# Kernel tuning notes

Hardware: AMD Instinct MI355X
Metric: run time of the kernel (lower is better)

The kernel has to match this reference:

```python
import jax, jax.numpy as jnp
import numpy as np

B, S_IMG, S_TXT, H, D = 1, 2048, 512, 24, 128
HID = H * D  # 3072
S_TOT = S_TXT + S_IMG
IP_SCALE = 1.0
EPS = 1e-5


def setup_inputs() -> dict:
    key = jax.random.key(0)
    ks = jax.random.split(key, 16)
    r = lambda k, s: jax.random.normal(k, s, dtype=jnp.float32)
    w = lambda k, s: r(k, s) * 0.02
    theta = r(ks[15], (S_TOT, D))  # rotary angles over joint sequence
    z = lambda: jnp.zeros((HID,), jnp.float32)
    return dict(
        hidden_states=r(ks[0], (B, S_IMG, HID)),
        encoder_hidden_states=r(ks[1], (B, S_TXT, HID)),
        image_emb=r(ks[2], (B, 4, HID)),
        rope_cos=jnp.cos(theta), rope_sin=jnp.sin(theta),
        Wq=w(ks[3], (HID, HID)), bq=z(),
        Wk=w(ks[4], (HID, HID)), bk=z(),
        Wv=w(ks[5], (HID, HID)), bv=z(),
        Waq=w(ks[6], (HID, HID)), baq=z(),
        Wak=w(ks[7], (HID, HID)), bak=z(),
        Wav=w(ks[8], (HID, HID)), bav=z(),
        Wk_ip=w(ks[9], (HID, HID)),
        Wv_ip=w(ks[10], (HID, HID)),
        Wo=w(ks[11], (HID, HID)), bo=z(),
        Wao=w(ks[12], (HID, HID)), bao=z(),
    )


def _heads(x):  # [B,S,HID] -> [B,H,S,D]
    return x.reshape(x.shape[0], x.shape[1], H, D).transpose(0, 2, 1, 3)


def _unheads(x):  # [B,H,S,D] -> [B,S,HID]
    return x.transpose(0, 2, 1, 3).reshape(x.shape[0], x.shape[2], HID)


def _rmsnorm(x):  # over last dim, no affine (RMSNorm(128, affine=False))
    return x * jax.lax.rsqrt(jnp.mean(x * x, axis=-1, keepdims=True) + EPS)


def _rope(x, cos, sin):  # diffusers apply_rotary_emb, use_real, interleaved pairs
    xp = x.reshape(*x.shape[:-1], D // 2, 2)
    rot = jnp.stack([-xp[..., 1], xp[..., 0]], axis=-1).reshape(x.shape)
    return x * cos + rot * sin  # cos/sin [S,D] broadcast over [B,H,S,D]


def _sdpa(q, k, v):
    s = jnp.einsum('bhqd,bhkd->bhqk', q, k) / jnp.sqrt(jnp.asarray(D, q.dtype))
    return jnp.einsum('bhqk,bhkd->bhqd', jax.nn.softmax(s, axis=-1), v)


def _forward(hidden_states, encoder_hidden_states, image_emb, rope_cos, rope_sin,
             Wq, bq, Wk, bk, Wv, bv, Waq, baq, Wak, bak, Wav, bav,
             Wk_ip, Wv_ip, Wo, bo, Wao, bao):
    # main QKV over image-latent tokens
    q = _rmsnorm(_heads(hidden_states @ Wq.T + bq))
    k = _rmsnorm(_heads(hidden_states @ Wk.T + bk))
    v = _heads(hidden_states @ Wv.T + bv)
    # IP-adapter cross attention (query = latent q, kv from image_emb)
    k_ip = _rmsnorm(_heads(image_emb @ Wk_ip.T))
    v_ip = _heads(image_emb @ Wv_ip.T)
    ip_out = _unheads(_sdpa(q, k_ip, v_ip))  # [B,S_IMG,HID]
    # encoder (text) QKV, concat text-first as in Flux
    eq = _rmsnorm(_heads(encoder_hidden_states @ Waq.T + baq))
    ek = _rmsnorm(_heads(encoder_hidden_states @ Wak.T + bak))
    ev = _heads(encoder_hidden_states @ Wav.T + bav)
    q = jnp.concatenate([eq, q], axis=2)
    k = jnp.concatenate([ek, k], axis=2)
    v = jnp.concatenate([ev, v], axis=2)
    q = _rope(q, rope_cos, rope_sin)
    k = _rope(k, rope_cos, rope_sin)
    out = _unheads(_sdpa(q, k, v))  # [B,S_TOT,HID]
    enc_out, hid_out = out[:, :S_TXT], out[:, S_TXT:]
    hid_out = hid_out + IP_SCALE * ip_out
    hid_out = hid_out @ Wo.T + bo   # to_out[0] (+ identity dropout)
    enc_out = enc_out @ Wao.T + bao  # to_add_out
    return hid_out, enc_out


def reference(hidden_states, encoder_hidden_states, image_emb, rope_cos, rope_sin,
              Wq, bq, Wk, bk, Wv, bv, Waq, baq, Wak, bak, Wav, bav,
              Wk_ip, Wv_ip, Wo, bo, Wao, bao):
    return _forward(hidden_states, encoder_hidden_states, image_emb, rope_cos, rope_sin,
                    Wq, bq, Wk, bk, Wv, bv, Waq, baq, Wak, bak, Wav, bav,
                    Wk_ip, Wv_ip, Wo, bo, Wao, bao)
```

## Files before the change

kernel.cpp:

```cpp
#include <hip/hip_runtime.h>

typedef __bf16 bf16;
typedef __bf16 bf16x2 __attribute__((ext_vector_type(2)));
typedef __bf16 bf16x4 __attribute__((ext_vector_type(4)));
typedef __bf16 bf16x8 __attribute__((ext_vector_type(8)));
typedef float  f32x4  __attribute__((ext_vector_type(4)));

#define H_    24
#define D_    128
#define HID_  3072
#define SIMG_ 2048
#define STXT_ 512
#define STOT_ 2560
#define EPS_  1e-5f
#define SCALE_ 0.08838834764831845f
#define HH_   ((size_t)HID_*HID_)

typedef __attribute__((address_space(3))) unsigned int lds_uint;
typedef const __attribute__((address_space(1))) unsigned int glb_uint;
__device__ __forceinline__ void gll16(const void* g, void* l){
  __builtin_amdgcn_global_load_lds((glb_uint*)g, (lds_uint*)l, 16, 0, 0);
}

__device__ inline bf16x8 frag8f(const float* __restrict__ p){
  const f32x4 a = *(const f32x4*)p;
  const f32x4 b = *(const f32x4*)(p + 4);
  bf16x8 r;
  r[0]=(bf16)a[0]; r[1]=(bf16)a[1]; r[2]=(bf16)a[2]; r[3]=(bf16)a[3];
  r[4]=(bf16)b[0]; r[5]=(bf16)b[1]; r[6]=(bf16)b[2]; r[7]=(bf16)b[3];
  return r;
}

__device__ __forceinline__ void cvt8(const float* __restrict__ s, bf16* __restrict__ d, int i){
  const f32x4 a = *(const f32x4*)(s + i);
  const f32x4 b = *(const f32x4*)(s + i + 4);
  bf16x8 o;
  o[0]=(bf16)a[0]; o[1]=(bf16)a[1]; o[2]=(bf16)a[2]; o[3]=(bf16)a[3];
  o[4]=(bf16)b[0]; o[5]=(bf16)b[1]; o[6]=(bf16)b[2]; o[7]=(bf16)b[3];
  *(bf16x8*)(d + i) = o;
}

#define CONV_BLK 2048
__global__ __launch_bounds__(256) void k_prep(
    const float* __restrict__ HS, const float* __restrict__ ENC,
    const float* __restrict__ W0, const float* __restrict__ W1,
    const float* __restrict__ W2, const float* __restrict__ W3,
    const float* __restrict__ W4, const float* __restrict__ W5,
    const float* __restrict__ W6, const float* __restrict__ W7,
    const float* __restrict__ IMG,
    const float* __restrict__ Wkip, const float* __restrict__ Wvip,
    bf16* __restrict__ HSb, bf16* __restrict__ ENCb, bf16* __restrict__ Wb8,
    float* __restrict__ Kip, float* __restrict__ Vip)
{
  __shared__ float tile[4][128];
  const int bx = (int)blockIdx.x;
  const int t = (int)threadIdx.x;
  if (bx < 48){
    const bool isV = (bx >= 24);
    const int h = bx % 24;
    const float* Wm = isV ? Wvip : Wkip;
    const int w = t >> 6, l = t & 63;
    const int lr = l & 15, lg = l >> 4;
    const int col0 = h*128 + w*32;
    f32x4 acc0 = {}, acc1 = {};
    const float* arow = IMG + (size_t)((lr < 4) ? lr : 0)*HID_;
    const float* wr0 = Wm + (size_t)(col0 + lr)*HID_;
    const float* wr1 = Wm + (size_t)(col0 + 16 + lr)*HID_;
    for (int k0 = 0; k0 < HID_; k0 += 32){
      const bf16x8 af = frag8f(arow + k0 + lg*8);
      acc0 = __builtin_amdgcn_mfma_f32_16x16x32_bf16(af, frag8f(wr0 + k0 + lg*8), acc0, 0, 0, 0);
      acc1 = __builtin_amdgcn_mfma_f32_16x16x32_bf16(af, frag8f(wr1 + k0 + lg*8), acc1, 0, 0, 0);
    }
    if (lg == 0){
      #pragma unroll
      for (int r = 0; r < 4; r++){
        tile[r][w*32 + lr]      = acc0[r];
        tile[r][w*32 + 16 + lr] = acc1[r];
      }
    }
    __syncthreads();
    if (isV){
      const int e = t*2;
      const int j = e >> 7, d = e & 127;
      Vip[(size_t)(h*4 + j)*D_ + d]     = tile[j][d];
      Vip[(size_t)(h*4 + j)*D_ + d + 1] = tile[j][d + 1];
    } else {
      const float v0 = tile[w][2*l], v1 = tile[w][2*l + 1];
      float ss = v0*v0 + v1*v1;
      #pragma unroll
      for (int m = 1; m < 64; m <<= 1) ss += __shfl_xor(ss, m);
      const float rk = rsqrtf(ss*(1.0f/128.0f) + EPS_);
      Kip[(size_t)(h*4 + w)*D_ + 2*l]     = v0*rk;
      Kip[(size_t)(h*4 + w)*D_ + 2*l + 1] = v1*rk;
    }
  } else {
    for (int c = bx - 48; c < 20352; c += CONV_BLK){
      const float* s; bf16* d; int base;
      if (c < 1536){ s = HS;  d = HSb;  base = c*4096; }
      else if (c < 1920){ s = ENC; d = ENCb; base = (c - 1536)*4096; }
      else {
        const int idx = c - 1920;
        const int wi = idx / 2304;
        s = (wi==0)?W0:(wi==1)?W1:(wi==2)?W2:(wi==3)?W3:(wi==4)?W4:(wi==5)?W5:(wi==6)?W6:W7;
        d = Wb8 + (size_t)wi*HH_;
        base = (idx % 2304)*4096;
      }
      const int i = base + t*16;
      cvt8(s, d, i);
      cvt8(s, d, i + 8);
    }
  }
}

#define MFMA_ __builtin_amdgcn_mfma_f32_16x16x32_bf16
#define MM(bfr, n) \
    acc[0][n]=MFMA_(af0,bfr,acc[0][n],0,0,0); acc[1][n]=MFMA_(af1,bfr,acc[1][n],0,0,0); \
    acc[2][n]=MFMA_(af2,bfr,acc[2][n],0,0,0); acc[3][n]=MFMA_(af3,bfr,acc[3][n],0,0,0);
#define WAIT6  asm volatile("s_waitcnt vmcnt(6)" ::: "memory")
#define WAIT0  asm volatile("s_waitcnt vmcnt(0)" ::: "memory")
#define NOWAIT (void)0

__device__ __forceinline__ void gemm8_core(
    const bf16* __restrict__ A, const bf16* __restrict__ W,
    int mb, int nb,
    f32x4 (&acc)[4][4],
    bf16 (&Al)[3][128][64],
    bf16 (&Bl)[3][256][64])
{
  const int t = (int)threadIdx.x;
  const int w = t >> 6, l = t & 63;
  const int lr = l & 15, lg = l >> 4;
  const int wr = w >> 2, wc = w & 3;
  const int srow = t >> 3;
  const int soff = ((t & 7) ^ (srow & 7)) * 8;

  const bf16* Abase = A + (size_t)(mb + srow)*HID_ + soff;
  const bf16* Wbase = W + (size_t)(nb + srow)*HID_ + soff;

#define SA(buf, tt, i) gll16(Abase + (size_t)(i)*64*HID_ + (tt)*64, &Al[buf][0][0] + (i)*4096 + t*8)
#define SB(buf, tt, i) gll16(Wbase + (size_t)(i)*64*HID_ + (tt)*64, &Bl[buf][0][0] + (i)*4096 + t*8)

  const int arow_ = wr*64 + lr;
  const int brow_ = wc*64 + lr;
  const int sx = lr & 7;

  SA(0,0,0); SA(0,0,1); SB(0,0,0); SB(0,0,1); SB(0,0,2); SB(0,0,3);
  SA(1,1,0); SA(1,1,1); SB(1,1,0); SB(1,1,1); SB(1,1,2); SB(1,1,3);
  WAIT6;
  __builtin_amdgcn_s_barrier();

#define TILE(C, NXT, TT, PRE, TW)                                            \
  {                                                                          \
    const int s0_ = (lg^sx)*8, s1_ = ((4+lg)^sx)*8;                          \
    bf16x8 af0,af1,af2,af3,b0,b1;                                            \
    af0=*(const bf16x8*)&Al[C][arow_   ][s0_];                               \
    af1=*(const bf16x8*)&Al[C][arow_+16][s0_];                               \
    af2=*(const bf16x8*)&Al[C][arow_+32][s0_];                               \
    af3=*(const bf16x8*)&Al[C][arow_+48][s0_];                               \
    b0 =*(const bf16x8*)&Bl[C][brow_   ][s0_];                               \
    b1 =*(const bf16x8*)&Bl[C][brow_+16][s0_];                               \
    if (PRE){ SA(NXT,(TT)+2,0); SA(NXT,(TT)+2,1); }                          \
    __builtin_amdgcn_s_setprio(1); MM(b0,0) MM(b1,1)                         \
    __builtin_amdgcn_s_setprio(0);                                           \
    b0 =*(const bf16x8*)&Bl[C][brow_+32][s0_];                               \
    b1 =*(const bf16x8*)&Bl[C][brow_+48][s0_];                               \
    if (PRE){ SB(NXT,(TT)+2,0); SB(NXT,(TT)+2,1); }                          \
    __builtin_amdgcn_s_setprio(1); MM(b0,2) MM(b1,3)                         \
    __builtin_amdgcn_s_setprio(0);                                           \
    af0=*(const bf16x8*)&Al[C][arow_   ][s1_];                               \
    af1=*(const bf16x8*)&Al[C][arow_+16][s1_];                               \
    af2=*(const bf16x8*)&Al[C][arow_+32][s1_];                               \
    af3=*(const bf16x8*)&Al[C][arow_+48][s1_];                               \
    b0 =*(const bf16x8*)&Bl[C][brow_   ][s1_];                               \
    b1 =*(const bf16x8*)&Bl[C][brow_+16][s1_];                               \
    if (PRE){ SB(NXT,(TT)+2,2); SB(NXT,(TT)+2,3); }                          \
    __builtin_amdgcn_s_setprio(1); MM(b0,0) MM(b1,1)                         \
    __builtin_amdgcn_s_setprio(0);                                           \
    b0 =*(const bf16x8*)&Bl[C][brow_+32][s1_];                               \
    b1 =*(const bf16x8*)&Bl[C][brow_+48][s1_];                               \
    __builtin_amdgcn_s_setprio(1); MM(b0,2) MM(b1,3)                         \
    __builtin_amdgcn_s_setprio(0);                                           \
    TW;                                                                      \
    __builtin_amdgcn_s_barrier();                                            \
  }

  for (int base = 0; base < 45; base += 3){
    TILE(0, 2, base,   true, WAIT6);
    TILE(1, 0, base+1, true, WAIT6);
    TILE(2, 1, base+2, true, WAIT6);
  }
  TILE(0, 2, 45, true,  WAIT6);
  TILE(1, 0, 46, false, WAIT0);
  TILE(2, 1, 47, false, NOWAIT);
#undef TILE
#undef SA
#undef SB
}

__global__ __launch_bounds__(512, 1) void k_gemm8_qkv(
    const bf16* __restrict__ Ahid, const bf16* __restrict__ Aenc,
    const bf16* __restrict__ Wb,
    const float* bq, const float* bk, const float* bv,
    const float* baq, const float* bak, const float* bav,
    bf16* Cq, bf16* Ck, bf16* Cv, bf16* Ceq, bf16* Cek, bf16* Cev)
{
  __shared__ __align__(16) bf16 Al[3][128][64];
  __shared__ __align__(16) bf16 Bl[3][256][64];
  const int lin = (int)blockIdx.x;
  const int work = (lin & 7)*90 + (lin >> 3);
  const int mt = work / 36;
  const int ct = work % 36;
  const int which = ct % 3;
  const int nb = (ct/3)*256;
  const int enc = (mt >= 16) ? 1 : 0;
  const int mb = (enc ? (mt - 16) : mt)*128;
  const bf16* A = enc ? Aenc : Ahid;
  const int widx = which + enc*3;
  const bf16* W = Wb + (size_t)widx*HH_;
  const float* bias = (which==0) ? (enc?baq:bq) : (which==1) ? (enc?bak:bk) : (enc?bav:bv);
  bf16* Cm = (which==0) ? (enc?Ceq:Cq) : (which==1) ? (enc?Cek:Ck) : (enc?Cev:Cv);

  f32x4 acc[4][4] = {};
  gemm8_core(A, W, mb, nb, acc, Al, Bl);

  const int w = (int)(threadIdx.x >> 6), l = (int)(threadIdx.x & 63u);
  const int lr = l & 15, lg = l >> 4;
  const int wr = w >> 2, wc = w & 3;
  #pragma unroll
  for (int nf = 0; nf < 4; nf++){
    const int col = nb + wc*64 + nf*16 + lr;
    const float bvl = bias[col];
    #pragma unroll
    for (int m = 0; m < 4; m++){
      #pragma unroll
      for (int r = 0; r < 4; r++){
        const int row = mb + wr*64 + m*16 + lg*4 + r;
        Cm[(size_t)row*HID_ + col] = (bf16)(acc[m][nf][r] + bvl);
      }
    }
  }
}

__global__ __launch_bounds__(512, 1) void k_gemm8_out(
    const bf16* __restrict__ Ahid, const bf16* __restrict__ Aenc,
    const bf16* __restrict__ Wb,
    const float* bo, const float* bao, float* __restrict__ outp)
{
  __shared__ __align__(16) bf16 Al[3][128][64];
  __shared__ __align__(16) bf16 Bl[3][256][64];
  const int lin = (int)blockIdx.x;
  const int work = (lin & 7)*30 + (lin >> 3);
  const int mt = work / 12;
  const int nb = (work % 12)*256;
  const int enc = (mt >= 16) ? 1 : 0;
  const int mb = (enc ? (mt - 16) : mt)*128;
  const bf16* A = enc ? Aenc : Ahid;
  const bf16* W = Wb + (size_t)(enc ? 7 : 6)*HH_;
  const float* bias = enc ? bao : bo;
  float* C = outp + (enc ? (size_t)SIMG_*HID_ : 0);

  f32x4 acc[4][4] = {};
  gemm8_core(A, W, mb, nb, acc, Al, Bl);

  const int w = (int)(threadIdx.x >> 6), l = (int)(threadIdx.x & 63u);
  const int lr = l & 15, lg = l >> 4;
  const int wr = w >> 2, wc = w & 3;
  #pragma unroll
  for (int nf = 0; nf < 4; nf++){
    const int col = nb + wc*64 + nf*16 + lr;
    const float bvl = bias[col];
    #pragma unroll
    for (int m = 0; m < 4; m++){
      #pragma unroll
      for (int r = 0; r < 4; r++){
        const int row = mb + wr*64 + m*16 + lg*4 + r;
        C[(size_t)row*HID_ + col] = acc[m][nf][r] + bvl;
      }
    }
  }
}

#define FIN_BLK 2048
__global__ __launch_bounds__(256) void k_finish_qk2(
    const bf16* __restrict__ rawQ, const bf16* __restrict__ rawK,
    const bf16* __restrict__ rawEQ, const bf16* __restrict__ rawEK,
    const float* __restrict__ cosT, const float* __restrict__ sinT,
    const float* __restrict__ Kip, const float* __restrict__ Vip,
    bf16* __restrict__ Qh, bf16* __restrict__ Kh, bf16* __restrict__ ipOut)
{
  const int wv = (int)(threadIdx.x >> 6);
  const int l = (int)(threadIdx.x & 63u);
  const int d0 = 2*l, d1 = 2*l + 1;
  for (int b = (int)blockIdx.x; b < 15360; b += FIN_BLK){
    const int wid = b*4 + wv;
    const int s = wid / H_;
    const int h = wid % H_;
    const bf16 *sq_, *sk_;
    if (s < STXT_){
      const size_t off = (size_t)s*HID_ + h*D_;
      sq_ = rawEQ + off; sk_ = rawEK + off;
    } else {
      const size_t off = (size_t)(s - STXT_)*HID_ + h*D_;
      sq_ = rawQ + off; sk_ = rawK + off;
    }
    float q0 = sq_[d0], q1 = sq_[d1];
    float k0 = sk_[d0], k1 = sk_[d1];
    float ssq = q0*q0 + q1*q1;
    float ssk = k0*k0 + k1*k1;
    #pragma unroll
    for (int m = 1; m < 64; m <<= 1){ ssq += __shfl_xor(ssq, m); ssk += __shfl_xor(ssk, m); }
    const float rq = rsqrtf(ssq*(1.0f/128.0f) + EPS_);
    const float rk = rsqrtf(ssk*(1.0f/128.0f) + EPS_);
    q0 *= rq; q1 *= rq; k0 *= rk; k1 *= rk;
    const float c0 = cosT[(size_t)s*D_ + d0], c1 = cosT[(size_t)s*D_ + d1];
    const float s0 = sinT[(size_t)s*D_ + d0], s1 = sinT[(size_t)s*D_ + d1];
    const float qo0 = q0*c0 - q1*s0, qo1 = q1*c1 + q0*s1;
    const float ko0 = k0*c0 - k1*s0, ko1 = k1*c1 + k0*s1;
    const size_t qoff = ((size_t)h*STOT_ + s)*D_ + d0;
    Qh[qoff] = (bf16)qo0; Qh[qoff + 1] = (bf16)qo1;
    Kh[qoff] = (bf16)ko0; Kh[qoff + 1] = (bf16)ko1;

    if (s >= STXT_){
      const float* kb = Kip + (size_t)h*4*D_;
      const float* vb = Vip + (size_t)h*4*D_;
      float sc[4];
      #pragma unroll
      for (int j = 0; j < 4; j++) sc[j] = q0*kb[j*D_ + d0] + q1*kb[j*D_ + d1];
      #pragma unroll
      for (int m = 1; m < 64; m <<= 1){
        #pragma unroll
        for (int j = 0; j < 4; j++) sc[j] += __shfl_xor(sc[j], m);
      }
      const float mx = fmaxf(fmaxf(sc[0], sc[1]), fmaxf(sc[2], sc[3]));
      float p[4], ps = 0.f;
      #pragma unroll
      for (int j = 0; j < 4; j++){ p[j] = __expf((sc[j] - mx)*SCALE_); ps += p[j]; }
      const float inv = 1.0f/ps;
      float o0 = 0.f, o1 = 0.f;
      #pragma unroll
      for (int j = 0; j < 4; j++){ o0 += p[j]*vb[j*D_ + d0]; o1 += p[j]*vb[j*D_ + d1]; }
      const size_t dst = (size_t)(s - STXT_)*HID_ + h*D_;
      ipOut[dst + d0] = (bf16)(o0*inv);
      ipOut[dst + d1] = (bf16)(o1*inv);
    }
  }
}

__global__ __launch_bounds__(256) void k_vtrans(
    const bf16* __restrict__ rawV, const bf16* __restrict__ rawEV,
    bf16* __restrict__ Vt)
{
  __shared__ bf16 lt[128*130];
  const int t = (int)threadIdx.x;
  const int stile = (int)blockIdx.x*128;
  const int h = (int)blockIdx.y;
  #pragma unroll
  for (int i = 0; i < 8; i++){
    const int sl = i*16 + (t >> 4);
    const int s = stile + sl;
    const bf16* src = (s < STXT_) ? (rawEV + (size_t)s*HID_) : (rawV + (size_t)(s - STXT_)*HID_);
    const bf16x8 v = *(const bf16x8*)(src + h*D_ + (t & 15)*8);
    #pragma unroll
    for (int j = 0; j < 8; j++) lt[((t & 15)*8 + j)*130 + sl] = v[j];
  }
  __syncthreads();
  #pragma unroll
  for (int j = 0; j < 4; j++){
    const int d = j*32 + (t >> 3);
    const int s0 = (t & 7)*16;
    bf16x8 a, b;
    #pragma unroll
    for (int k = 0; k < 4; k++){
      const bf16x2 p = *(const bf16x2*)(lt + d*130 + s0 + 2*k);
      a[2*k] = p[0]; a[2*k+1] = p[1];
    }
    #pragma unroll
    for (int k = 0; k < 4; k++){
      const bf16x2 p = *(const bf16x2*)(lt + d*130 + s0 + 8 + 2*k);
      b[2*k] = p[0]; b[2*k+1] = p[1];
    }
    bf16* dst = Vt + ((size_t)h*D_ + d)*STOT_ + stile + s0;
    *(bf16x8*)dst = a;
    *(bf16x8*)(dst + 8) = b;
  }
}

__global__ __launch_bounds__(256, 2) void k_flash3(
    const bf16* __restrict__ Q, const bf16* __restrict__ K,
    const bf16* __restrict__ Vt, const bf16* __restrict__ ipOut,
    bf16* __restrict__ attnOut)
{
  __shared__ __align__(16) bf16 Ks[2][64*128];
  __shared__ __align__(16) bf16 Vs[2][128*64];
  __shared__ __align__(16) bf16 plds[4][32*64];
  const int t = (int)threadIdx.x;
  const int w = t >> 6, l = t & 63;
  const int lr = l & 15, lg = l >> 4;
  const int lin = (int)blockIdx.x;
  const int work = (lin & 7)*60 + (lin >> 3);
  const int h = work / 20;
  const int qbase = (work % 20)*128 + w*32;
  const bf16* Qh = Q  + (size_t)h*STOT_*D_;
  const bf16* Kh = K  + (size_t)h*STOT_*D_;
  const bf16* Vh = Vt + (size_t)h*D_*STOT_;

  bf16x8 qf[2][4];
  #pragma unroll
  for (int qt = 0; qt < 2; qt++)
    #pragma unroll
    for (int kk = 0; kk < 4; kk++)
      qf[qt][kk] = *(const bf16x8*)(Qh + (size_t)(qbase + qt*16 + lr)*D_ + kk*32 + lg*8);

  f32x4 acc[2][8] = {};
  float mrun[2] = {-3.0e38f, -3.0e38f}, lrun[2] = {0.f, 0.f};

  const int krow = t >> 4, kslot = t & 15;
  const int vrow = t >> 3, vslot = t & 7;

  auto STAGE = [&](int buf, int kv){
    #pragma unroll
    for (int i = 0; i < 4; i++){
      const int r = i*16 + krow;
      gll16(Kh + (size_t)(kv + r)*D_ + ((kslot ^ (r & 7))*8),
            (void*)(&Ks[buf][0] + (size_t)t*8 + i*2048));
    }
    #pragma unroll
    for (int i = 0; i < 4; i++){
      const int r = i*32 + vrow;
      gll16(Vh + (size_t)r*STOT_ + kv + ((vslot ^ (r & 7))*8),
            (void*)(&Vs[buf][0] + (size_t)t*8 + i*2048));
    }
  };

  STAGE(0, 0);
  __syncthreads();
  int cur = 0;
  for (int kv = 0; kv < STOT_; kv += 64){
    if (kv + 64 < STOT_) STAGE(cur ^ 1, kv + 64);

    f32x4 st[2][4] = {};
    #pragma unroll
    for (int tt = 0; tt < 4; tt++){
      const int kr = tt*16 + lr;
      #pragma unroll
      for (int kk = 0; kk < 4; kk++){
        const bf16x8 kf = *(const bf16x8*)(&Ks[cur][0] + kr*128 + (((kk*4 + lg) ^ (kr & 7))*8));
        st[0][tt] = __builtin_amdgcn_mfma_f32_16x16x32_bf16(kf, qf[0][kk], st[0][tt], 0, 0, 0);
        st[1][tt] = __builtin_amdgcn_mfma_f32_16x16x32_bf16(kf, qf[1][kk], st[1][tt], 0, 0, 0);
      }
    }
    #pragma unroll
    for (int qt = 0; qt < 2; qt++){
      const int q = qt*16 + lr;
      float sv[4][4];
      float vmax = -3.0e38f;
      #pragma unroll
      for (int tt = 0; tt < 4; tt++)
        #pragma unroll
        for (int r = 0; r < 4; r++){ const float x = st[qt][tt][r]*SCALE_; sv[tt][r] = x; vmax = fmaxf(vmax, x); }
      vmax = fmaxf(vmax, __shfl_xor(vmax, 16));
      vmax = fmaxf(vmax, __shfl_xor(vmax, 32));
      const bool grow = __any(vmax > mrun[qt] + 8.0f);
      float mnew = mrun[qt];
      if (grow){
        mnew = fmaxf(mrun[qt], vmax);
        const float alpha = __expf(mrun[qt] - mnew);
        lrun[qt] *= alpha;
        #pragma unroll
        for (int n = 0; n < 8; n++)
          #pragma unroll
          for (int r = 0; r < 4; r++) acc[qt][n][r] *= alpha;
        mrun[qt] = mnew;
      }
      float rs = 0.f;
      #pragma unroll
      for (int tt = 0; tt < 4; tt++){
        bf16x4 pq;
        #pragma unroll
        for (int r = 0; r < 4; r++){
          const float p = __expf(sv[tt][r] - mnew);
          rs += p;
          pq[r] = (bf16)p;
        }
        *(bf16x4*)(&plds[w][q*64 + (((tt*2 + (lg >> 1)) ^ (q & 7))*8) + (lg & 1)*4]) = pq;
      }
      rs += __shfl_xor(rs, 16);
      rs += __shfl_xor(rs, 32);
      lrun[qt] += rs;
    }
    #pragma unroll
    for (int ks = 0; ks < 2; ks++){
      const bf16x8 pb0 = *(const bf16x8*)(&plds[w][(lr)*64      + (((ks*4 + lg) ^ (lr & 7))*8)]);
      const bf16x8 pb1 = *(const bf16x8*)(&plds[w][(16 + lr)*64 + (((ks*4 + lg) ^ (lr & 7))*8)]);
      #pragma unroll
      for (int n = 0; n < 8; n++){
        const int vr = n*16 + lr;
        const bf16x8 vf = *(const bf16x8*)(&Vs[cur][0] + vr*64 + (((ks*4 + lg) ^ (vr & 7))*8));
        acc[0][n] = __builtin_amdgcn_mfma_f32_16x16x32_bf16(vf, pb0, acc[0][n], 0, 0, 0);
        acc[1][n] = __builtin_amdgcn_mfma_f32_16x16x32_bf16(vf, pb1, acc[1][n], 0, 0, 0);
      }
    }
    __syncthreads();
    cur ^= 1;
  }
  const bool hid = (qbase >= STXT_);
  #pragma unroll
  for (int qt = 0; qt < 2; qt++){
    const float inv = 1.0f/lrun[qt];
    const int row = qbase + qt*16 + lr;
    #pragma unroll
    for (int n = 0; n < 8; n++){
      const size_t cbase = (size_t)row*HID_ + h*D_ + n*16 + lg*4;
      if (hid){
        const bf16x4 ip = *(const bf16x4*)(ipOut + (size_t)(row - STXT_)*HID_ + h*D_ + n*16 + lg*4);
        bf16x4 o;
        #pragma unroll
        for (int r = 0; r < 4; r++) o[r] = (bf16)(acc[qt][n][r]*inv + (float)ip[r]);
        *(bf16x4*)(attnOut + cbase) = o;
      } else {
        bf16x4 o;
        #pragma unroll
        for (int r = 0; r < 4; r++) o[r] = (bf16)(acc[qt][n][r]*inv);
        *(bf16x4*)(attnOut + cbase) = o;
      }
    }
  }
}

extern "C" void kernel_launch(void* const* d_in, const int* in_sizes, int n_in,
                              void* d_out, int out_size, void* d_ws, size_t ws_size,
                              hipStream_t stream)
{
  const float* HS   = (const float*)d_in[0];
  const float* ENC  = (const float*)d_in[1];
  const float* IMG  = (const float*)d_in[2];
  const float* COS  = (const float*)d_in[3];
  const float* SIN  = (const float*)d_in[4];
  const float* Wq   = (const float*)d_in[5];  const float* bq  = (const float*)d_in[6];
  const float* Wk   = (const float*)d_in[7];  const float* bk  = (const float*)d_in[8];
  const float* Wv   = (const float*)d_in[9];  const float* bv  = (const float*)d_in[10];
  const float* Waq  = (const float*)d_in[11]; const float* baq = (const float*)d_in[12];
  const float* Wak  = (const float*)d_in[13]; const float* bak = (const float*)d_in[14];
  const float* Wav  = (const float*)d_in[15]; const float* bav = (const float*)d_in[16];
  const float* Wkip = (const float*)d_in[17]; const float* Wvip= (const float*)d_in[18];
  const float* Wo   = (const float*)d_in[19]; const float* bo  = (const float*)d_in[20];
  const float* Wao  = (const float*)d_in[21]; const float* bao = (const float*)d_in[22];

  char* wsb = (char*)d_ws;
  size_t off = 0;
  auto alloc = [&](size_t bytes) -> char* {
    char* p = wsb + off; off += (bytes + 255) & ~((size_t)255); return p;
  };
  bf16* rawQ   = (bf16*)alloc((size_t)SIMG_*HID_*2);
  bf16* rawK   = (bf16*)alloc((size_t)SIMG_*HID_*2);
  bf16* rawV   = (bf16*)alloc((size_t)SIMG_*HID_*2);
  bf16* rawEQ  = (bf16*)alloc((size_t)STXT_*HID_*2);
  bf16* rawEK  = (bf16*)alloc((size_t)STXT_*HID_*2);
  bf16* rawEV  = (bf16*)alloc((size_t)STXT_*HID_*2);
  bf16* Qb     = (bf16*)alloc((size_t)H_*STOT_*D_*2);
  bf16* Kb     = (bf16*)alloc((size_t)H_*STOT_*D_*2);
  bf16* Vtb    = (bf16*)alloc((size_t)H_*STOT_*D_*2);
  bf16* AOUT   = (bf16*)alloc((size_t)STOT_*HID_*2);
  bf16* IPOUT  = (bf16*)alloc((size_t)SIMG_*HID_*2);
  float* KIPF  = (float*)alloc((size_t)H_*4*D_*4);
  float* VIPF  = (float*)alloc((size_t)H_*4*D_*4);
  bf16* HSb    = (bf16*)alloc((size_t)SIMG_*HID_*2);
  bf16* ENCb   = (bf16*)alloc((size_t)STXT_*HID_*2);
  bf16* Wb8    = (bf16*)alloc((size_t)8*HH_*2);

  dim3 blk(256);
  dim3 blk512(512);
  k_prep<<<dim3(48 + CONV_BLK), blk, 0, stream>>>(HS, ENC, Wq, Wk, Wv, Waq, Wak, Wav, Wo, Wao,
                                                  IMG, Wkip, Wvip, HSb, ENCb, Wb8, KIPF, VIPF);
  k_gemm8_qkv<<<dim3(720), blk512, 0, stream>>>(HSb, ENCb, Wb8,
                                                bq, bk, bv, baq, bak, bav,
                                                rawQ, rawK, rawV, rawEQ, rawEK, rawEV);
  k_finish_qk2<<<dim3(FIN_BLK), blk, 0, stream>>>(rawQ, rawK, rawEQ, rawEK, COS, SIN,
                                                  KIPF, VIPF, Qb, Kb, IPOUT);
  k_vtrans<<<dim3(20,24), blk, 0, stream>>>(rawV, rawEV, Vtb);
  k_flash3<<<dim3(480), blk, 0, stream>>>(Qb, Kb, Vtb, IPOUT, AOUT);
  float* outp = (float*)d_out;
  k_gemm8_out<<<dim3(240), blk512, 0, stream>>>(AOUT + (size_t)STXT_*HID_, AOUT, Wb8, bo, bao, outp);
}
```

Measured before the change: 534.1 us.

## Replace QKV GEMM with 128x192 tile, 256-thread, two-blocks-per-CU kernel

Replaces the 512-thread 128x256-tile QKV projection GEMM with a new 256-thread kernel that computes 128x192 tiles using a 32-wide K step, a triple-buffered LDS pipeline and a new swizzled LDS layout. The grid becomes 960 blocks with two blocks per CU, so the tile count divides more evenly across CUs and occupancy rises. Each wave holds a 64x96 accumulator, which adds register pressure, and the shorter K step doubles the number of barriers per tile.

```diff
diff --git a/kernel.cpp b/kernel.cpp
--- a/kernel.cpp
+++ b/kernel.cpp
@@ -113,12 +113,127 @@
 }
 
 #define MFMA_ __builtin_amdgcn_mfma_f32_16x16x32_bf16
+#define WAIT6  asm volatile("s_waitcnt vmcnt(6)" ::: "memory")
+#define WAIT5  asm volatile("s_waitcnt vmcnt(5)" ::: "memory")
+#define WAIT0  asm volatile("s_waitcnt vmcnt(0)" ::: "memory")
+#define NOWAIT (void)0
+
+__global__ __launch_bounds__(256, 2) void k_gemm192_qkv(
+    const bf16* __restrict__ Ahid, const bf16* __restrict__ Aenc,
+    const bf16* __restrict__ Wb,
+    const float* bq, const float* bk, const float* bv,
+    const float* baq, const float* bak, const float* bav,
+    bf16* Cq, bf16* Ck, bf16* Cv, bf16* Ceq, bf16* Cek, bf16* Cev)
+{
+  __shared__ __align__(16) bf16 Al[3][4096];
+  __shared__ __align__(16) bf16 Bl[3][6144];
+  const int t = (int)threadIdx.x;
+  const int w = t >> 6, l = t & 63;
+  const int lr = l & 15, lg = l >> 4;
+  const int wr = w >> 1, wc = w & 1;
+
+  const int lin = (int)blockIdx.x;
+  const int work = (lin & 7)*120 + (lin >> 3);
+  const int mt = work / 48;
+  const int ct = work % 48;
+  const int which = ct % 3;
+  const int nb = (ct/3)*192;
+  const int enc = (mt >= 16) ? 1 : 0;
+  const int mb = (enc ? (mt - 16) : mt)*128;
+  const bf16* A = enc ? Aenc : Ahid;
+  const int widx = which + enc*3;
+  const bf16* W = Wb + (size_t)widx*HH_;
+  const float* bias = (which==0) ? (enc?baq:bq) : (which==1) ? (enc?bak:bk) : (enc?bav:bv);
+  bf16* Cm = (which==0) ? (enc?Ceq:Cq) : (which==1) ? (enc?Cek:Ck) : (enc?Cev:Cv);
+
+  const int lA0 = t >> 3,          uA0 = (t & 7) ^ (lA0 & 7);
+  const int gA1 = t + 256, lA1 = gA1 >> 3, uA1 = (gA1 & 7) ^ (lA1 & 7);
+  const bf16* Asrc0 = A + (size_t)(mb + 2*lA0 + (uA0 >> 2))*HID_ + (uA0 & 3)*8;
+  const bf16* Asrc1 = A + (size_t)(mb + 2*lA1 + (uA1 >> 2))*HID_ + (uA1 & 3)*8;
+  const int lB0 = t >> 3,          uB0 = (t & 7) ^ (lB0 & 7);
+  const int gB1 = t + 256, lB1 = gB1 >> 3, uB1 = (gB1 & 7) ^ (lB1 & 7);
+  const int gB2 = t + 512, lB2 = gB2 >> 3, uB2 = (gB2 & 7) ^ (lB2 & 7);
+  const bf16* Bsrc0 = W + (size_t)(nb + 2*lB0 + (uB0 >> 2))*HID_ + (uB0 & 3)*8;
+  const bf16* Bsrc1 = W + (size_t)(nb + 2*lB1 + (uB1 >> 2))*HID_ + (uB1 & 3)*8;
+  const bf16* Bsrc2 = W + (size_t)(nb + 2*lB2 + (uB2 >> 2))*HID_ + (uB2 & 3)*8;
+
+#define SA192(buf, TT) { gll16(Asrc0 + (TT)*32, &Al[buf][0] + t*8); \
+                         gll16(Asrc1 + (TT)*32, &Al[buf][0] + 2048 + t*8); }
+#define SB192(buf, TT) { gll16(Bsrc0 + (TT)*32, &Bl[buf][0] + t*8); \
+                         gll16(Bsrc1 + (TT)*32, &Bl[buf][0] + 2048 + t*8); \
+                         gll16(Bsrc2 + (TT)*32, &Bl[buf][0] + 4096 + t*8); }
+
+  const int gx = ((((lr & 1) << 2) | lg) ^ ((lr >> 1) & 7)) * 8;
+  const int baseA = (wr*32 + (lr >> 1))*64 + gx;
+  const int baseB = (wc*48 + (lr >> 1))*64 + gx;
+
+  f32x4 acc[4][6] = {};
+
+#define MMB(bb, n) \
+    acc[0][n]=MFMA_(a0,bb,acc[0][n],0,0,0); acc[1][n]=MFMA_(a1,bb,acc[1][n],0,0,0); \
+    acc[2][n]=MFMA_(a2,bb,acc[2][n],0,0,0); acc[3][n]=MFMA_(a3,bb,acc[3][n],0,0,0);
+
+#define TILE192(C, NXT, TT, PRE, TW)                                         \
+  {                                                                          \
+    bf16x8 a0,a1,a2,a3,b0,b1,b2;                                             \
+    a0 = *(const bf16x8*)(&Al[C][0] + baseA);                                \
+    a1 = *(const bf16x8*)(&Al[C][0] + baseA + 512);                          \
+    a2 = *(const bf16x8*)(&Al[C][0] + baseA + 1024);                         \
+    a3 = *(const bf16x8*)(&Al[C][0] + baseA + 1536);                         \
+    b0 = *(const bf16x8*)(&Bl[C][0] + baseB);                                \
+    b1 = *(const bf16x8*)(&Bl[C][0] + baseB + 512);                          \
+    b2 = *(const bf16x8*)(&Bl[C][0] + baseB + 1024);                         \
+    if (PRE){ SA192(NXT, (TT)+2); }                                          \
+    __builtin_amdgcn_s_setprio(1);                                           \
+    MMB(b0,0) MMB(b1,1) MMB(b2,2)                                            \
+    __builtin_amdgcn_s_setprio(0);                                           \
+    b0 = *(const bf16x8*)(&Bl[C][0] + baseB + 1536);                         \
+    b1 = *(const bf16x8*)(&Bl[C][0] + baseB + 2048);                         \
+    b2 = *(const bf16x8*)(&Bl[C][0] + baseB + 2560);                         \
+    if (PRE){ SB192(NXT, (TT)+2); }                                          \
+    __builtin_amdgcn_s_setprio(1);                                           \
+    MMB(b0,3) MMB(b1,4) MMB(b2,5)                                            \
+    __builtin_amdgcn_s_setprio(0);                                           \
+    TW;                                                                      \
+    __builtin_amdgcn_s_barrier();                                            \
+  }
+
+  SA192(0,0); SB192(0,0);
+  SA192(1,1); SB192(1,1);
+  WAIT5;
+  __builtin_amdgcn_s_barrier();
+
+  for (int base = 0; base < 93; base += 3){
+    TILE192(0, 2, base,   true, WAIT5);
+    TILE192(1, 0, base+1, true, WAIT5);
+    TILE192(2, 1, base+2, true, WAIT5);
+  }
+  TILE192(0, 2, 93, true,  WAIT5);
+  TILE192(1, 0, 94, false, WAIT0);
+  TILE192(2, 1, 95, false, NOWAIT);
+#undef TILE192
+#undef MMB
+#undef SA192
+#undef SB192
+
+  #pragma unroll
+  for (int n = 0; n < 6; n++){
+    const int col = nb + wc*96 + n*16 + lr;
+    const float bvl = bias[col];
+    #pragma unroll
+    for (int m = 0; m < 4; m++){
+      #pragma unroll
+      for (int r = 0; r < 4; r++){
+        const int row = mb + wr*64 + m*16 + lg*4 + r;
+        Cm[(size_t)row*HID_ + col] = (bf16)(acc[m][n][r] + bvl);
+      }
+    }
+  }
+}
+
 #define MM(bfr, n) \
     acc[0][n]=MFMA_(af0,bfr,acc[0][n],0,0,0); acc[1][n]=MFMA_(af1,bfr,acc[1][n],0,0,0); \
     acc[2][n]=MFMA_(af2,bfr,acc[2][n],0,0,0); acc[3][n]=MFMA_(af3,bfr,acc[3][n],0,0,0);
-#define WAIT6  asm volatile("s_waitcnt vmcnt(6)" ::: "memory")
-#define WAIT0  asm volatile("s_waitcnt vmcnt(0)" ::: "memory")
-#define NOWAIT (void)0
 
 __device__ __forceinline__ void gemm8_core(
     const bf16* __restrict__ A, const bf16* __restrict__ W,
@@ -197,50 +312,6 @@
 #undef SB
 }
 
-__global__ __launch_bounds__(512, 1) void k_gemm8_qkv(
-    const bf16* __restrict__ Ahid, const bf16* __restrict__ Aenc,
-    const bf16* __restrict__ Wb,
-    const float* bq, const float* bk, const float* bv,
-    const float* baq, const float* bak, const float* bav,
-    bf16* Cq, bf16* Ck, bf16* Cv, bf16* Ceq, bf16* Cek, bf16* Cev)
-{
-  __shared__ __align__(16) bf16 Al[3][128][64];
-  __shared__ __align__(16) bf16 Bl[3][256][64];
-  const int lin = (int)blockIdx.x;
-  const int work = (lin & 7)*90 + (lin >> 3);
-  const int mt = work / 36;
-  const int ct = work % 36;
-  const int which = ct % 3;
-  const int nb = (ct/3)*256;
-  const int enc = (mt >= 16) ? 1 : 0;
-  const int mb = (enc ? (mt - 16) : mt)*128;
-  const bf16* A = enc ? Aenc : Ahid;
-  const int widx = which + enc*3;
-  const bf16* W = Wb + (size_t)widx*HH_;
-  const float* bias = (which==0) ? (enc?baq:bq) : (which==1) ? (enc?bak:bk) : (enc?bav:bv);
-  bf16* Cm = (which==0) ? (enc?Ceq:Cq) : (which==1) ? (enc?Cek:Ck) : (enc?Cev:Cv);
-
-  f32x4 acc[4][4] = {};
-  gemm8_core(A, W, mb, nb, acc, Al, Bl);
-
-  const int w = (int)(threadIdx.x >> 6), l = (int)(threadIdx.x & 63u);
-  const int lr = l & 15, lg = l >> 4;
-  const int wr = w >> 2, wc = w & 3;
-  #pragma unroll
-  for (int nf = 0; nf < 4; nf++){
-    const int col = nb + wc*64 + nf*16 + lr;
-    const float bvl = bias[col];
-    #pragma unroll
-    for (int m = 0; m < 4; m++){
-      #pragma unroll
-      for (int r = 0; r < 4; r++){
-        const int row = mb + wr*64 + m*16 + lg*4 + r;
-        Cm[(size_t)row*HID_ + col] = (bf16)(acc[m][nf][r] + bvl);
-      }
-    }
-  }
-}
-
 __global__ __launch_bounds__(512, 1) void k_gemm8_out(
     const bf16* __restrict__ Ahid, const bf16* __restrict__ Aenc,
     const bf16* __restrict__ Wb,
@@ -572,9 +643,9 @@
   dim3 blk512(512);
   k_prep<<<dim3(48 + CONV_BLK), blk, 0, stream>>>(HS, ENC, Wq, Wk, Wv, Waq, Wak, Wav, Wo, Wao,
                                                   IMG, Wkip, Wvip, HSb, ENCb, Wb8, KIPF, VIPF);
-  k_gemm8_qkv<<<dim3(720), blk512, 0, stream>>>(HSb, ENCb, Wb8,
-                                                bq, bk, bv, baq, bak, bav,
-                                                rawQ, rawK, rawV, rawEQ, rawEK, rawEV);
+  k_gemm192_qkv<<<dim3(960), blk, 0, stream>>>(HSb, ENCb, Wb8,
+                                               bq, bk, bv, baq, bak, bav,
+                                               rawQ, rawK, rawV, rawEQ, rawEK, rawEV);
   k_finish_qk2<<<dim3(FIN_BLK), blk, 0, stream>>>(rawQ, rawK, rawEQ, rawEK, COS, SIN,
                                                   KIPF, VIPF, Qb, Kb, IPOUT);
   k_vtrans<<<dim3(20,24), blk, 0, stream>>>(rawV, rawEV, Vtb);
```

After: 513.0 us (median of 2 runs). -3.9%, faster.

## Replace QKV GEMM with 256x192 tile, 4-wave kernel and larger per-wave accumulators

Applied to the files above, without the earlier changes.

The QKV projection GEMM now uses a new kernel with 256x192 output tiles, 256 threads (4 waves) and a 128x96 per-wave accumulator block (8x6 MFMA tiles), replacing the 128x256 tile, 512-thread kernel. K is consumed in 32-wide steps with a triple-buffered global_load_lds pipeline and a new swizzled LDS layout. The larger per-wave tile raises arithmetic intensity per LDS read and cuts global traffic per FLOP. In exchange it uses far more accumulator registers, launches 480 blocks instead of 720 (fewer than two waves of blocks over the CUs), and runs twice as many barrier-synchronised K steps.

```diff
diff --git a/kernel.cpp b/kernel.cpp
--- a/kernel.cpp
+++ b/kernel.cpp
@@ -113,12 +113,136 @@
 }
 
 #define MFMA_ __builtin_amdgcn_mfma_f32_16x16x32_bf16
+#define WAIT7  asm volatile("s_waitcnt vmcnt(7)" ::: "memory")
+#define WAIT6  asm volatile("s_waitcnt vmcnt(6)" ::: "memory")
+#define WAIT0  asm volatile("s_waitcnt vmcnt(0)" ::: "memory")
+#define NOWAIT (void)0
+
+__global__ __launch_bounds__(256, 1) void k_gemm256x192_qkv(
+    const bf16* __restrict__ Ahid, const bf16* __restrict__ Aenc,
+    const bf16* __restrict__ Wb,
+    const float* bq, const float* bk, const float* bv,
+    const float* baq, const float* bak, const float* bav,
+    bf16* Cq, bf16* Ck, bf16* Cv, bf16* Ceq, bf16* Cek, bf16* Cev)
+{
+  __shared__ __align__(16) bf16 Al[3][8192];
+  __shared__ __align__(16) bf16 Bl[3][6144];
+  const int t = (int)threadIdx.x;
+  const int w = t >> 6, l = t & 63;
+  const int lr = l & 15, lg = l >> 4;
+  const int wr = w >> 1, wc = w & 1;
+
+  const int lin = (int)blockIdx.x;
+  const int work = (lin & 7)*60 + (lin >> 3);
+  const int mt = work / 48;
+  const int ct = work % 48;
+  const int which = ct % 3;
+  const int nb = (ct/3)*192;
+  const int enc = (mt >= 8) ? 1 : 0;
+  const int mb = (enc ? (mt - 8) : mt)*256;
+  const bf16* A = enc ? Aenc : Ahid;
+  const int widx = which + enc*3;
+  const bf16* W = Wb + (size_t)widx*HH_;
+  const float* bias = (which==0) ? (enc?baq:bq) : (which==1) ? (enc?bak:bk) : (enc?bav:bv);
+  bf16* Cm = (which==0) ? (enc?Ceq:Cq) : (which==1) ? (enc?Cek:Ck) : (enc?Cev:Cv);
+
+  const bf16* Asrc[4];
+  const bf16* Bsrc[3];
+  #pragma unroll
+  for (int i = 0; i < 4; i++){
+    const int gd = t + 256*i, ln = gd >> 3, u = (gd & 7) ^ (ln & 7);
+    Asrc[i] = A + (size_t)(mb + 2*ln + (u >> 2))*HID_ + (u & 3)*8;
+  }
+  #pragma unroll
+  for (int i = 0; i < 3; i++){
+    const int gd = t + 256*i, ln = gd >> 3, u = (gd & 7) ^ (ln & 7);
+    Bsrc[i] = W + (size_t)(nb + 2*ln + (u >> 2))*HID_ + (u & 3)*8;
+  }
+
+#define SAQ(buf, TT) { gll16(Asrc[0] + (TT)*32, &Al[buf][0] + t*8); \
+                       gll16(Asrc[1] + (TT)*32, &Al[buf][0] + 2048 + t*8); \
+                       gll16(Asrc[2] + (TT)*32, &Al[buf][0] + 4096 + t*8); \
+                       gll16(Asrc[3] + (TT)*32, &Al[buf][0] + 6144 + t*8); }
+#define SBQ(buf, TT) { gll16(Bsrc[0] + (TT)*32, &Bl[buf][0] + t*8); \
+                       gll16(Bsrc[1] + (TT)*32, &Bl[buf][0] + 2048 + t*8); \
+                       gll16(Bsrc[2] + (TT)*32, &Bl[buf][0] + 4096 + t*8); }
+
+  const int gx = ((((lr & 1) << 2) | lg) ^ ((lr >> 1) & 7)) * 8;
+  const int baseA = (wr*64 + (lr >> 1))*64 + gx;
+  const int baseB = (wc*48 + (lr >> 1))*64 + gx;
+
+  f32x4 acc[8][6] = {};
+
+#define MM6(am, m) \
+    acc[m][0]=MFMA_(am,b0,acc[m][0],0,0,0); acc[m][1]=MFMA_(am,b1,acc[m][1],0,0,0); \
+    acc[m][2]=MFMA_(am,b2,acc[m][2],0,0,0); acc[m][3]=MFMA_(am,b3,acc[m][3],0,0,0); \
+    acc[m][4]=MFMA_(am,b4,acc[m][4],0,0,0); acc[m][5]=MFMA_(am,b5,acc[m][5],0,0,0);
+
+#define TILEQ(C, TT, PRE, TW)                                                \
+  {                                                                          \
+    bf16x8 a0,a1,a2,a3,b0,b1,b2,b3,b4,b5;                                    \
+    a0 = *(const bf16x8*)(&Al[C][0] + baseA);                                \
+    a1 = *(const bf16x8*)(&Al[C][0] + baseA + 512);                          \
+    a2 = *(const bf16x8*)(&Al[C][0] + baseA + 1024);                         \
+    a3 = *(const bf16x8*)(&Al[C][0] + baseA + 1536);                         \
+    b0 = *(const bf16x8*)(&Bl[C][0] + baseB);                                \
+    b1 = *(const bf16x8*)(&Bl[C][0] + baseB + 512);                          \
+    b2 = *(const bf16x8*)(&Bl[C][0] + baseB + 1024);                         \
+    b3 = *(const bf16x8*)(&Bl[C][0] + baseB + 1536);                         \
+    b4 = *(const bf16x8*)(&Bl[C][0] + baseB + 2048);                         \
+    b5 = *(const bf16x8*)(&Bl[C][0] + baseB + 2560);                         \
+    if (PRE){ SAQ(((C)+2)%3, (TT)+2); }                                      \
+    __builtin_amdgcn_s_setprio(1);                                           \
+    MM6(a0,0) MM6(a1,1) MM6(a2,2) MM6(a3,3)                                  \
+    __builtin_amdgcn_s_setprio(0);                                           \
+    a0 = *(const bf16x8*)(&Al[C][0] + baseA + 2048);                         \
+    a1 = *(const bf16x8*)(&Al[C][0] + baseA + 2560);                         \
+    a2 = *(const bf16x8*)(&Al[C][0] + baseA + 3072);                         \
+    a3 = *(const bf16x8*)(&Al[C][0] + baseA + 3584);                         \
+    if (PRE){ SBQ(((C)+2)%3, (TT)+2); }                                      \
+    __builtin_amdgcn_s_setprio(1);                                           \
+    MM6(a0,4) MM6(a1,5) MM6(a2,6) MM6(a3,7)                                  \
+    __builtin_amdgcn_s_setprio(0);                                           \
+    TW;                                                                      \
+    __builtin_amdgcn_s_barrier();                                            \
+  }
+
+  SAQ(0,0); SBQ(0,0);
+  SAQ(1,1); SBQ(1,1);
+  WAIT7;
+  __builtin_amdgcn_s_barrier();
+
+  for (int base = 0; base < 93; base += 3){
+    TILEQ(0, base,   true, WAIT7);
+    TILEQ(1, base+1, true, WAIT7);
+    TILEQ(2, base+2, true, WAIT7);
+  }
+  TILEQ(0, 93, true,  WAIT7);
+  TILEQ(1, 94, false, WAIT0);
+  TILEQ(2, 95, false, NOWAIT);
+#undef TILEQ
+#undef MM6
+#undef SAQ
+#undef SBQ
+
+  #pragma unroll
+  for (int n = 0; n < 6; n++){
+    const int col = nb + wc*96 + n*16 + lr;
+    const float bvl = bias[col];
+    #pragma unroll
+    for (int m = 0; m < 8; m++){
+      #pragma unroll
+      for (int r = 0; r < 4; r++){
+        const int row = mb + wr*128 + m*16 + lg*4 + r;
+        Cm[(size_t)row*HID_ + col] = (bf16)(acc[m][n][r] + bvl);
+      }
+    }
+  }
+}
+
 #define MM(bfr, n) \
     acc[0][n]=MFMA_(af0,bfr,acc[0][n],0,0,0); acc[1][n]=MFMA_(af1,bfr,acc[1][n],0,0,0); \
     acc[2][n]=MFMA_(af2,bfr,acc[2][n],0,0,0); acc[3][n]=MFMA_(af3,bfr,acc[3][n],0,0,0);
-#define WAIT6  asm volatile("s_waitcnt vmcnt(6)" ::: "memory")
-#define WAIT0  asm volatile("s_waitcnt vmcnt(0)" ::: "memory")
-#define NOWAIT (void)0
 
 __device__ __forceinline__ void gemm8_core(
     const bf16* __restrict__ A, const bf16* __restrict__ W,
@@ -197,50 +321,6 @@
 #undef SB
 }
 
-__global__ __launch_bounds__(512, 1) void k_gemm8_qkv(
-    const bf16* __restrict__ Ahid, const bf16* __restrict__ Aenc,
-    const bf16* __restrict__ Wb,
-    const float* bq, const float* bk, const float* bv,
-    const float* baq, const float* bak, const float* bav,
-    bf16* Cq, bf16* Ck, bf16* Cv, bf16* Ceq, bf16* Cek, bf16* Cev)
-{
-  __shared__ __align__(16) bf16 Al[3][128][64];
-  __shared__ __align__(16) bf16 Bl[3][256][64];
-  const int lin = (int)blockIdx.x;
-  const int work = (lin & 7)*90 + (lin >> 3);
-  const int mt = work / 36;
-  const int ct = work % 36;
-  const int which = ct % 3;
-  const int nb = (ct/3)*256;
-  const int enc = (mt >= 16) ? 1 : 0;
-  const int mb = (enc ? (mt - 16) : mt)*128;
-  const bf16* A = enc ? Aenc : Ahid;
-  const int widx = which + enc*3;
-  const bf16* W = Wb + (size_t)widx*HH_;
-  const float* bias = (which==0) ? (enc?baq:bq) : (which==1) ? (enc?bak:bk) : (enc?bav:bv);
-  bf16* Cm = (which==0) ? (enc?Ceq:Cq) : (which==1) ? (enc?Cek:Ck) : (enc?Cev:Cv);
-
-  f32x4 acc[4][4] = {};
-  gemm8_core(A, W, mb, nb, acc, Al, Bl);
-
-  const int w = (int)(threadIdx.x >> 6), l = (int)(threadIdx.x & 63u);
-  const int lr = l & 15, lg = l >> 4;
-  const int wr = w >> 2, wc = w & 3;
-  #pragma unroll
-  for (int nf = 0; nf < 4; nf++){
-    const int col = nb + wc*64 + nf*16 + lr;
-    const float bvl = bias[col];
-    #pragma unroll
-    for (int m = 0; m < 4; m++){
-      #pragma unroll
-      for (int r = 0; r < 4; r++){
-        const int row = mb + wr*64 + m*16 + lg*4 + r;
-        Cm[(size_t)row*HID_ + col] = (bf16)(acc[m][nf][r] + bvl);
-      }
-    }
-  }
-}
-
 __global__ __launch_bounds__(512, 1) void k_gemm8_out(
     const bf16* __restrict__ Ahid, const bf16* __restrict__ Aenc,
     const bf16* __restrict__ Wb,
@@ -572,9 +652,9 @@
   dim3 blk512(512);
   k_prep<<<dim3(48 + CONV_BLK), blk, 0, stream>>>(HS, ENC, Wq, Wk, Wv, Waq, Wak, Wav, Wo, Wao,
                                                   IMG, Wkip, Wvip, HSb, ENCb, Wb8, KIPF, VIPF);
-  k_gemm8_qkv<<<dim3(720), blk512, 0, stream>>>(HSb, ENCb, Wb8,
-                                                bq, bk, bv, baq, bak, bav,
-                                                rawQ, rawK, rawV, rawEQ, rawEK, rawEV);
+  k_gemm256x192_qkv<<<dim3(480), blk, 0, stream>>>(HSb, ENCb, Wb8,
+                                                   bq, bk, bv, baq, bak, bav,
+                                                   rawQ, rawK, rawV, rawEQ, rawEK, rawEV);
   k_finish_qk2<<<dim3(FIN_BLK), blk, 0, stream>>>(rawQ, rawK, rawEQ, rawEK, COS, SIN,
                                                   KIPF, VIPF, Qb, Kb, IPOUT);
   k_vtrans<<<dim3(20,24), blk, 0, stream>>>(rawV, rawEV, Vtb);
```

New measurement: 526.2 us. No clear change (-1.5%).
